# Kernel tuning notes

Hardware: AMD Instinct MI355X
Metric: run time of the kernel (lower is better)

## Reference

```python
import jax, jax.numpy as jnp
import numpy as np

BALL_SIZE = 128


def setup_inputs() -> dict:
    key = jax.random.key(0)
    kq, kk, kv = jax.random.split(key, 3)
    B, H, n, Dh = 4, 16, 8192, 64
    q = jax.random.normal(kq, (B, H, n, Dh), dtype=jnp.float32)
    k = jax.random.normal(kk, (B, H, n, Dh), dtype=jnp.float32)
    v = jax.random.normal(kv, (B, H, n, Dh), dtype=jnp.float32)
    return {"q": q, "k": k, "v": v}


def reference(q, k, v) -> jnp.ndarray:
    # Block-local (ball) attention: attention computed independently within
    # each contiguous ball of size BALL_SIZE along the sequence dim.
    B, H, n, Dh = q.shape
    bs = BALL_SIZE
    m = n // bs
    # (B, H, m, bs, D) -- split seq into balls; attention only within a ball.
    qb = q.reshape(B, H, m, bs, Dh)
    kb = k.reshape(B, H, m, bs, Dh)
    vb = v.reshape(B, H, m, bs, Dh)
    scale = 1.0 / jnp.sqrt(jnp.asarray(Dh, dtype=q.dtype))
    scores = jnp.einsum('bhmqd,bhmkd->bhmqk', qb, kb) * scale  # (B,H,m,bs,bs)
    attn = jax.nn.softmax(scores, axis=-1)
    out = jnp.einsum('bhmqk,bhmkd->bhmqd', attn, vb)
    return out.reshape(B, H, n, Dh)
```

## Files before the change

kernel.cpp:

```cpp
#include <hip/hip_runtime.h>

typedef _Float16 half2_t __attribute__((ext_vector_type(2)));
typedef _Float16 half4_t __attribute__((ext_vector_type(4)));
typedef _Float16 half8_t __attribute__((ext_vector_type(8)));
typedef __fp16   fp16x2  __attribute__((ext_vector_type(2)));
typedef float    f32x16  __attribute__((ext_vector_type(16)));

#define BS 128
#define DH 64

static __device__ __forceinline__ half2_t pkrtz(float x, float y) {
  fp16x2 t = __builtin_amdgcn_cvt_pkrtz(x, y);
  return __builtin_bit_cast(half2_t, t);
}
static __device__ __forceinline__ unsigned pkrtz_u(float x, float y) {
  fp16x2 t = __builtin_amdgcn_cvt_pkrtz(x, y);
  return __builtin_bit_cast(unsigned, t);
}

static __device__ __forceinline__ half8_t cvt8(const float4 a, const float4 b) {
  half2_t h0 = pkrtz(a.x, a.y);
  half2_t h1 = pkrtz(a.z, a.w);
  half2_t h2 = pkrtz(b.x, b.y);
  half2_t h3 = pkrtz(b.z, b.w);
  half4_t lo = __builtin_shufflevector(h0, h1, 0, 1, 2, 3);
  half4_t hi = __builtin_shufflevector(h2, h3, 0, 1, 2, 3);
  return __builtin_shufflevector(lo, hi, 0, 1, 2, 3, 4, 5, 6, 7);
}

static __device__ __forceinline__ half8_t h8_from(unsigned r0, unsigned r1,
                                                  unsigned r2, unsigned r3) {
  half2_t h0 = __builtin_bit_cast(half2_t, r0);
  half2_t h1 = __builtin_bit_cast(half2_t, r1);
  half2_t h2 = __builtin_bit_cast(half2_t, r2);
  half2_t h3 = __builtin_bit_cast(half2_t, r3);
  half4_t lo = __builtin_shufflevector(h0, h1, 0, 1, 2, 3);
  half4_t hi = __builtin_shufflevector(h2, h3, 0, 1, 2, 3);
  return __builtin_shufflevector(lo, hi, 0, 1, 2, 3, 4, 5, 6, 7);
}

static __device__ __forceinline__ void plswap(unsigned x, unsigned y,
                                              unsigned& olo, unsigned& ohi) {
#if __has_builtin(__builtin_amdgcn_permlane32_swap)
  auto pr = __builtin_amdgcn_permlane32_swap((int)x, (int)y, false, false);
  unsigned tmp[2];
  __builtin_memcpy(tmp, &pr, 8);
  olo = tmp[0];
  ohi = tmp[1];
#else
  const int h = (threadIdx.x & 63) >> 5;
  unsigned xs = (unsigned)__shfl_xor((int)x, 32);
  unsigned ys = (unsigned)__shfl_xor((int)y, 32);
  olo = h ? ys : x;
  ohi = h ? y : xs;
#endif
}

static __device__ __forceinline__ int svt(int d) { return (d & 7) ^ ((d >> 2) & 7); }

__global__ __launch_bounds__(256) void ball_attn_kernel(
    const float* __restrict__ Q, const float* __restrict__ Kk,
    const float* __restrict__ V, float* __restrict__ O) {
  __shared__ __align__(16) _Float16 VT[2][DH * BS];

  const int tid  = threadIdx.x;
  const int w    = tid >> 6;
  const int grp  = w >> 1;
  const int wg   = w & 1;
  const int lane = tid & 63;
  const int ld   = lane & 31;
  const int hi   = lane >> 5;
  const int gtid = tid & 127;

  const int nwg = gridDim.x;
  const int bid = blockIdx.x;
  const int blk = (bid & 7) * (nwg >> 3) + (bid >> 3);

  const size_t base = ((size_t)blk * 2 + grp) * (BS * DH);
  const float* Qb = Q + base;
  const float* Kb = Kk + base;
  const float* Vb = V + base;
  float*       Ob = O + base;
  _Float16*    vt = VT[grp];

  {
    const int kgrp = gtid >> 4;
    const int d0   = (gtid & 15) * 4;
#pragma unroll
    for (int half = 0; half < 2; ++half) {
      float4 a[4], b[4];
#pragma unroll
      for (int it2 = 0; it2 < 4; ++it2) {
        const int keyA = 2 * kgrp + 16 * (half * 4 + it2);
        a[it2] = *(const float4*)(Vb + (size_t)keyA * DH + d0);
        b[it2] = *(const float4*)(Vb + (size_t)(keyA + 1) * DH + d0);
      }
#pragma unroll
      for (int it2 = 0; it2 < 4; ++it2) {
        const int keyA = 2 * kgrp + 16 * (half * 4 + it2);
        const float* ap = (const float*)&a[it2];
        const float* bp = (const float*)&b[it2];
#pragma unroll
        for (int j = 0; j < 4; ++j) {
          const int d = d0 + j;
          *(half2_t*)&vt[d * BS + (keyA ^ (svt(d) << 3))] = pkrtz(ap[j], bp[j]);
        }
      }
    }
  }

  __syncthreads();

#pragma unroll 1
  for (int qt = 0; qt < 2; ++qt) {
    const int qbase = 64 * wg + 32 * qt;

    half8_t bq[4];
    {
      float4 qa[4], qb[4];
#pragma unroll
      for (int ds = 0; ds < 4; ++ds) {
        const float* qp = Qb + (qbase + ld) * DH + ds * 16 + hi * 8;
        qa[ds] = *(const float4*)qp;
        qb[ds] = *(const float4*)(qp + 4);
      }
#pragma unroll
      for (int ds = 0; ds < 4; ++ds) bq[ds] = cvt8(qa[ds], qb[ds]);
    }

    f32x16 acc[4] = {};
#pragma unroll
    for (int kt = 0; kt < 4; ++kt) {
      float4 ka[4], kb[4];
#pragma unroll
      for (int ds = 0; ds < 4; ++ds) {
        const float* kp = Kb + (kt * 32 + ld) * DH + ds * 16 + hi * 8;
        ka[ds] = *(const float4*)kp;
        kb[ds] = *(const float4*)(kp + 4);
      }
#pragma unroll
      for (int ds = 0; ds < 4; ++ds) {
        const half8_t ak = cvt8(ka[ds], kb[ds]);
        acc[kt] = __builtin_amdgcn_mfma_f32_32x32x16_f16(ak, bq[ds], acc[kt], 0, 0, 0);
      }
    }

    float mx = acc[0][0];
#pragma unroll
    for (int kt = 0; kt < 4; ++kt)
#pragma unroll
      for (int r = 0; r < 16; ++r) mx = fmaxf(mx, acc[kt][r]);
    mx = fmaxf(mx, __shfl_xor(mx, 32));
    const float nmxs = -mx * 0.125f;
    float sm = 0.f;
#pragma unroll
    for (int kt = 0; kt < 4; ++kt)
#pragma unroll
      for (int r = 0; r < 16; ++r) {
        const float p = __expf(fmaf(acc[kt][r], 0.125f, nmxs));
        acc[kt][r] = p;
        sm += p;
      }
    sm += __shfl_xor(sm, 32);
    const float inv = __builtin_amdgcn_rcpf(sm);

    half8_t pf[8];
#pragma unroll
    for (int s = 0; s < 8; ++s) {
      const int kt = s >> 1;
      const int bA = 2 * (s & 1);
      const int bB = bA + 1;
      const unsigned A0 = pkrtz_u(acc[kt][4 * bA + 0] * inv, acc[kt][4 * bA + 1] * inv);
      const unsigned A1 = pkrtz_u(acc[kt][4 * bA + 2] * inv, acc[kt][4 * bA + 3] * inv);
      const unsigned B0 = pkrtz_u(acc[kt][4 * bB + 0] * inv, acc[kt][4 * bB + 1] * inv);
      const unsigned B1 = pkrtz_u(acc[kt][4 * bB + 2] * inv, acc[kt][4 * bB + 3] * inv);
      unsigned r0, r1, r2, r3;
      plswap(A0, B0, r0, r2);
      plswap(A1, B1, r1, r3);
      pf[s] = h8_from(r0, r1, r2, r3);
    }

    f32x16 o[2] = {};
#pragma unroll
    for (int dt = 0; dt < 2; ++dt) {
      const int row = dt * 32 + ld;
      const int sv  = svt(row) << 3;
#pragma unroll
      for (int s = 0; s < 8; ++s) {
        const half8_t vf = *(const half8_t*)&vt[row * BS + ((16 * s + 8 * hi) ^ sv)];
        o[dt] = __builtin_amdgcn_mfma_f32_32x32x16_f16(pf[s], vf, o[dt], 0, 0, 0);
      }
    }

#pragma unroll
    for (int dt = 0; dt < 2; ++dt)
#pragma unroll
      for (int r = 0; r < 16; ++r) {
        const int qrow = qbase + (r & 3) + 8 * (r >> 2) + 4 * hi;
        Ob[qrow * DH + dt * 32 + ld] = o[dt][r];
      }
  }
}

extern "C" void kernel_launch(void* const* d_in, const int* in_sizes, int n_in,
                              void* d_out, int out_size, void* d_ws, size_t ws_size,
                              hipStream_t stream) {
  const float* q = (const float*)d_in[0];
  const float* k = (const float*)d_in[1];
  const float* v = (const float*)d_in[2];
  float* out = (float*)d_out;
  const int nballs = in_sizes[0] / (BS * DH);
  ball_attn_kernel<<<dim3(nballs / 2), dim3(256), 0, stream>>>(q, k, v, out);
}
```

Measured before the change: 120.4 us.

## Process one ball per workgroup with one 32-query tile per wave

Changes the work split from two balls per 256-thread block (each wave doing two 32-query tiles in a loop) to one ball per block where each of the four waves handles a single 32-query tile. The grid doubles, shared memory per block halves, and the Q load is hoisted before the barrier so it overlaps the V transpose. This aims to raise occupancy and latency hiding. In exchange, each block now reads the full K of its ball once per wave, with four waves instead of two sharing it.

```diff
diff --git a/kernel.cpp b/kernel.cpp
--- a/kernel.cpp
+++ b/kernel.cpp
@@ -61,145 +61,134 @@
 __global__ __launch_bounds__(256) void ball_attn_kernel(
     const float* __restrict__ Q, const float* __restrict__ Kk,
     const float* __restrict__ V, float* __restrict__ O) {
-  __shared__ __align__(16) _Float16 VT[2][DH * BS];
+  __shared__ __align__(16) _Float16 VT[DH * BS];
 
   const int tid  = threadIdx.x;
   const int w    = tid >> 6;
-  const int grp  = w >> 1;
-  const int wg   = w & 1;
   const int lane = tid & 63;
   const int ld   = lane & 31;
   const int hi   = lane >> 5;
-  const int gtid = tid & 127;
 
   const int nwg = gridDim.x;
   const int bid = blockIdx.x;
-  const int blk = (bid & 7) * (nwg >> 3) + (bid >> 3);
-
-  const size_t base = ((size_t)blk * 2 + grp) * (BS * DH);
+  const int ball = (bid & 7) * (nwg >> 3) + (bid >> 3);
+
+  const size_t base = (size_t)ball * (BS * DH);
   const float* Qb = Q + base;
   const float* Kb = Kk + base;
   const float* Vb = V + base;
   float*       Ob = O + base;
-  _Float16*    vt = VT[grp];
 
   {
-    const int kgrp = gtid >> 4;
-    const int d0   = (gtid & 15) * 4;
-#pragma unroll
-    for (int half = 0; half < 2; ++half) {
-      float4 a[4], b[4];
-#pragma unroll
-      for (int it2 = 0; it2 < 4; ++it2) {
-        const int keyA = 2 * kgrp + 16 * (half * 4 + it2);
-        a[it2] = *(const float4*)(Vb + (size_t)keyA * DH + d0);
-        b[it2] = *(const float4*)(Vb + (size_t)(keyA + 1) * DH + d0);
+    const int kgrp = tid >> 4;
+    const int d0   = (tid & 15) * 4;
+    float4 a[4], b[4];
+#pragma unroll
+    for (int it = 0; it < 4; ++it) {
+      const int keyA = 2 * kgrp + 32 * it;
+      a[it] = *(const float4*)(Vb + (size_t)keyA * DH + d0);
+      b[it] = *(const float4*)(Vb + (size_t)(keyA + 1) * DH + d0);
+    }
+#pragma unroll
+    for (int it = 0; it < 4; ++it) {
+      const int keyA = 2 * kgrp + 32 * it;
+      const float* ap = (const float*)&a[it];
+      const float* bp = (const float*)&b[it];
+#pragma unroll
+      for (int j = 0; j < 4; ++j) {
+        const int d = d0 + j;
+        *(half2_t*)&VT[d * BS + (keyA ^ (svt(d) << 3))] = pkrtz(ap[j], bp[j]);
       }
-#pragma unroll
-      for (int it2 = 0; it2 < 4; ++it2) {
-        const int keyA = 2 * kgrp + 16 * (half * 4 + it2);
-        const float* ap = (const float*)&a[it2];
-        const float* bp = (const float*)&b[it2];
-#pragma unroll
-        for (int j = 0; j < 4; ++j) {
-          const int d = d0 + j;
-          *(half2_t*)&vt[d * BS + (keyA ^ (svt(d) << 3))] = pkrtz(ap[j], bp[j]);
-        }
-      }
-    }
+    }
+  }
+
+  const int qbase = 32 * w;
+  half8_t bq[4];
+  {
+    float4 qa[4], qb[4];
+#pragma unroll
+    for (int ds = 0; ds < 4; ++ds) {
+      const float* qp = Qb + (qbase + ld) * DH + ds * 16 + hi * 8;
+      qa[ds] = *(const float4*)qp;
+      qb[ds] = *(const float4*)(qp + 4);
+    }
+#pragma unroll
+    for (int ds = 0; ds < 4; ++ds) bq[ds] = cvt8(qa[ds], qb[ds]);
   }
 
   __syncthreads();
 
-#pragma unroll 1
-  for (int qt = 0; qt < 2; ++qt) {
-    const int qbase = 64 * wg + 32 * qt;
-
-    half8_t bq[4];
-    {
-      float4 qa[4], qb[4];
-#pragma unroll
-      for (int ds = 0; ds < 4; ++ds) {
-        const float* qp = Qb + (qbase + ld) * DH + ds * 16 + hi * 8;
-        qa[ds] = *(const float4*)qp;
-        qb[ds] = *(const float4*)(qp + 4);
-      }
-#pragma unroll
-      for (int ds = 0; ds < 4; ++ds) bq[ds] = cvt8(qa[ds], qb[ds]);
-    }
-
-    f32x16 acc[4] = {};
-#pragma unroll
-    for (int kt = 0; kt < 4; ++kt) {
-      float4 ka[4], kb[4];
-#pragma unroll
-      for (int ds = 0; ds < 4; ++ds) {
-        const float* kp = Kb + (kt * 32 + ld) * DH + ds * 16 + hi * 8;
-        ka[ds] = *(const float4*)kp;
-        kb[ds] = *(const float4*)(kp + 4);
-      }
-#pragma unroll
-      for (int ds = 0; ds < 4; ++ds) {
-        const half8_t ak = cvt8(ka[ds], kb[ds]);
-        acc[kt] = __builtin_amdgcn_mfma_f32_32x32x16_f16(ak, bq[ds], acc[kt], 0, 0, 0);
-      }
-    }
-
-    float mx = acc[0][0];
-#pragma unroll
-    for (int kt = 0; kt < 4; ++kt)
-#pragma unroll
-      for (int r = 0; r < 16; ++r) mx = fmaxf(mx, acc[kt][r]);
-    mx = fmaxf(mx, __shfl_xor(mx, 32));
-    const float nmxs = -mx * 0.125f;
-    float sm = 0.f;
-#pragma unroll
-    for (int kt = 0; kt < 4; ++kt)
-#pragma unroll
-      for (int r = 0; r < 16; ++r) {
-        const float p = __expf(fmaf(acc[kt][r], 0.125f, nmxs));
-        acc[kt][r] = p;
-        sm += p;
-      }
-    sm += __shfl_xor(sm, 32);
-    const float inv = __builtin_amdgcn_rcpf(sm);
-
-    half8_t pf[8];
+  f32x16 acc[4] = {};
+#pragma unroll
+  for (int kt = 0; kt < 4; ++kt) {
+    float4 ka[4], kb[4];
+#pragma unroll
+    for (int ds = 0; ds < 4; ++ds) {
+      const float* kp = Kb + (kt * 32 + ld) * DH + ds * 16 + hi * 8;
+      ka[ds] = *(const float4*)kp;
+      kb[ds] = *(const float4*)(kp + 4);
+    }
+#pragma unroll
+    for (int ds = 0; ds < 4; ++ds) {
+      const half8_t ak = cvt8(ka[ds], kb[ds]);
+      acc[kt] = __builtin_amdgcn_mfma_f32_32x32x16_f16(ak, bq[ds], acc[kt], 0, 0, 0);
+    }
+  }
+
+  float mx = acc[0][0];
+#pragma unroll
+  for (int kt = 0; kt < 4; ++kt)
+#pragma unroll
+    for (int r = 0; r < 16; ++r) mx = fmaxf(mx, acc[kt][r]);
+  mx = fmaxf(mx, __shfl_xor(mx, 32));
+  const float nmxs = -mx * 0.125f;
+  float sm = 0.f;
+#pragma unroll
+  for (int kt = 0; kt < 4; ++kt)
+#pragma unroll
+    for (int r = 0; r < 16; ++r) {
+      const float p = __expf(fmaf(acc[kt][r], 0.125f, nmxs));
+      acc[kt][r] = p;
+      sm += p;
+    }
+  sm += __shfl_xor(sm, 32);
+  const float inv = __builtin_amdgcn_rcpf(sm);
+
+  half8_t pf[8];
+#pragma unroll
+  for (int s = 0; s < 8; ++s) {
+    const int kt = s >> 1;
+    const int bA = 2 * (s & 1);
+    const int bB = bA + 1;
+    const unsigned A0 = pkrtz_u(acc[kt][4 * bA + 0] * inv, acc[kt][4 * bA + 1] * inv);
+    const unsigned A1 = pkrtz_u(acc[kt][4 * bA + 2] * inv, acc[kt][4 * bA + 3] * inv);
+    const unsigned B0 = pkrtz_u(acc[kt][4 * bB + 0] * inv, acc[kt][4 * bB + 1] * inv);
+    const unsigned B1 = pkrtz_u(acc[kt][4 * bB + 2] * inv, acc[kt][4 * bB + 3] * inv);
+    unsigned r0, r1, r2, r3;
+    plswap(A0, B0, r0, r2);
+    plswap(A1, B1, r1, r3);
+    pf[s] = h8_from(r0, r1, r2, r3);
+  }
+
+  f32x16 o[2] = {};
+#pragma unroll
+  for (int dt = 0; dt < 2; ++dt) {
+    const int row = dt * 32 + ld;
+    const int sv  = svt(row) << 3;
 #pragma unroll
     for (int s = 0; s < 8; ++s) {
-      const int kt = s >> 1;
-      const int bA = 2 * (s & 1);
-      const int bB = bA + 1;
-      const unsigned A0 = pkrtz_u(acc[kt][4 * bA + 0] * inv, acc[kt][4 * bA + 1] * inv);
-      const unsigned A1 = pkrtz_u(acc[kt][4 * bA + 2] * inv, acc[kt][4 * bA + 3] * inv);
-      const unsigned B0 = pkrtz_u(acc[kt][4 * bB + 0] * inv, acc[kt][4 * bB + 1] * inv);
-      const unsigned B1 = pkrtz_u(acc[kt][4 * bB + 2] * inv, acc[kt][4 * bB + 3] * inv);
-      unsigned r0, r1, r2, r3;
-      plswap(A0, B0, r0, r2);
-      plswap(A1, B1, r1, r3);
-      pf[s] = h8_from(r0, r1, r2, r3);
-    }
-
-    f32x16 o[2] = {};
-#pragma unroll
-    for (int dt = 0; dt < 2; ++dt) {
-      const int row = dt * 32 + ld;
-      const int sv  = svt(row) << 3;
-#pragma unroll
-      for (int s = 0; s < 8; ++s) {
-        const half8_t vf = *(const half8_t*)&vt[row * BS + ((16 * s + 8 * hi) ^ sv)];
-        o[dt] = __builtin_amdgcn_mfma_f32_32x32x16_f16(pf[s], vf, o[dt], 0, 0, 0);
-      }
-    }
-
-#pragma unroll
-    for (int dt = 0; dt < 2; ++dt)
-#pragma unroll
-      for (int r = 0; r < 16; ++r) {
-        const int qrow = qbase + (r & 3) + 8 * (r >> 2) + 4 * hi;
-        Ob[qrow * DH + dt * 32 + ld] = o[dt][r];
-      }
-  }
+      const half8_t vf = *(const half8_t*)&VT[row * BS + ((16 * s + 8 * hi) ^ sv)];
+      o[dt] = __builtin_amdgcn_mfma_f32_32x32x16_f16(pf[s], vf, o[dt], 0, 0, 0);
+    }
+  }
+
+#pragma unroll
+  for (int dt = 0; dt < 2; ++dt)
+#pragma unroll
+    for (int r = 0; r < 16; ++r) {
+      const int qrow = qbase + (r & 3) + 8 * (r >> 2) + 4 * hi;
+      Ob[qrow * DH + dt * 32 + ld] = o[dt][r];
+    }
 }
 
 extern "C" void kernel_launch(void* const* d_in, const int* in_sizes, int n_in,
@@ -210,5 +199,5 @@
   const float* v = (const float*)d_in[2];
   float* out = (float*)d_out;
   const int nballs = in_sizes[0] / (BS * DH);
-  ball_attn_kernel<<<dim3(nballs / 2), dim3(256), 0, stream>>>(q, k, v, out);
-}
+  ball_attn_kernel<<<dim3(nballs), dim3(256), 0, stream>>>(q, k, v, out);
+}
```

Measured after the change: 125.0 us. 3.8% more time.
